# Kernel tuning notes

Measured on AMD Instinct MI355X. Metric: run time of the kernel, lower is better.

The kernel has to match this reference:

```python
import jax, jax.numpy as jnp
import numpy as np

SQRT_HALF = np.float32(np.sqrt(0.5))


def _weight_norm(v, g):
    # torch weight_norm dim=0: per-output-row normalization, w = g * v / ||v||_row
    return (g / jnp.linalg.norm(v, axis=1))[:, None] * v


def setup_inputs() -> dict:
    key = jax.random.key(0)
    ks = jax.random.split(key, 6)
    B, L, C, E, H, W = 32, 1024, 1024, 1024, 14, 14
    return {
        "x": jax.random.normal(ks[0], (B, L, C), dtype=jnp.float32),
        "word_embed": jax.random.normal(ks[1], (B, L, E), dtype=jnp.float32),
        "conv_feats": jax.random.normal(ks[2], (B, E, H, W), dtype=jnp.float32),
        "in_v": jax.random.normal(ks[3], (E, C), dtype=jnp.float32) * np.float32(1.0 / np.sqrt(C)),
        "in_g": jnp.ones((E,), dtype=jnp.float32),
        "in_b": jnp.zeros((E,), dtype=jnp.float32),
        "out_v": jax.random.normal(ks[4], (C, E), dtype=jnp.float32) * np.float32(1.0 / np.sqrt(E)),
        "out_g": jnp.ones((C,), dtype=jnp.float32),
        "out_b": jnp.zeros((C,), dtype=jnp.float32),
    }


def reference(x, word_embed, conv_feats, in_v, in_g, in_b, out_v, out_g, out_b):
    # in_projection (weight-normed linear) + word_embed, scaled
    Wi = _weight_norm(in_v, in_g)                      # [E, C]
    h = (jnp.einsum('blc,ec->ble', x, Wi) + in_b + word_embed) * SQRT_HALF  # [B, L, E]

    B, E, H, W = conv_feats.shape
    n = H * W
    y = conv_feats.reshape(B, E, n)                    # [B, E, n]
    scores = jnp.einsum('ble,bev->blv', h, y)          # [B, L, n]
    attn = jax.nn.softmax(scores, axis=-1)             # [B, L, n]
    ctx = jnp.einsum('blv,bev->ble', attn, y)          # [B, L, E]
    ctx = ctx * jnp.asarray(n * np.sqrt(1.0 / n), dtype=ctx.dtype)  # = sqrt(n)

    # out_projection + residual, scaled
    Wo = _weight_norm(out_v, out_g)                    # [C, E]
    out = (jnp.einsum('ble,ce->blc', ctx, Wo) + out_b + x) * SQRT_HALF  # [B, L, C]
    return out, attn
```

## Files before the change

### kernel.cpp

```cpp
#include <hip/hip_runtime.h>
#include <hip/hip_bf16.h>

typedef unsigned short u16;
typedef _Float16 f16x8 __attribute__((ext_vector_type(8)));
typedef unsigned short u16x8 __attribute__((ext_vector_type(8)));
typedef float f32x4 __attribute__((ext_vector_type(4)));

#define SQHF 0.70710678118654752440f

__device__ __forceinline__ u16 f2h(float f) {
  const _Float16 h = (_Float16)f;
  return __builtin_bit_cast(u16, h);
}

template <int N>
__device__ __forceinline__ void vmwait() {
  asm volatile("s_waitcnt vmcnt(%0)" ::"i"(N) : "memory");
}

__device__ __forceinline__ void gload_lds16(const void* g, void* l) {
  __builtin_amdgcn_global_load_lds(
      (const __attribute__((address_space(1))) unsigned int*)g,
      (__attribute__((address_space(3))) unsigned int*)l, 16, 0, 0);
}

__device__ __forceinline__ float block_sum(float v) {
#pragma unroll
  for (int o = 32; o; o >>= 1) v += __shfl_xor(v, o);
  __shared__ float red[4];
  if ((threadIdx.x & 63) == 0) red[threadIdx.x >> 6] = v;
  __syncthreads();
  return red[0] + red[1] + red[2] + red[3];
}

__global__ void wnorm_t_kernel(const float* __restrict__ v, const float* __restrict__ g,
                               u16* __restrict__ wtf) {
  const int e = blockIdx.x;
  const float* vr = v + (long)e * 1024;
  float ss = 0.f;
  for (int c = threadIdx.x; c < 1024; c += 256) { float t = vr[c]; ss += t * t; }
  const float tot = block_sum(ss);
  const float scl = g[e] / sqrtf(tot);
  for (int c = threadIdx.x; c < 1024; c += 256) wtf[(long)c * 1024 + e] = f2h(vr[c] * scl);
}

__global__ void wnorm_kernel(const float* __restrict__ v, const float* __restrict__ g,
                             u16* __restrict__ w) {
  const int c = blockIdx.x;
  const float* vr = v + (long)c * 1024;
  float ss = 0.f;
  for (int e = threadIdx.x; e < 1024; e += 256) { float t = vr[e]; ss += t * t; }
  const float tot = block_sum(ss);
  const float scl = g[c] / sqrtf(tot);
  for (int e = threadIdx.x; e < 1024; e += 256) w[(long)c * 1024 + e] = f2h(vr[e] * scl);
}

__global__ void prep_y_kernel(const float* __restrict__ conv, const float* __restrict__ in_b,
                              u16* __restrict__ concat, float* __restrict__ rc) {
  const int b = blockIdx.x >> 4;
  const int e0 = (blockIdx.x & 15) << 6;
  __shared__ float tile[64 * 224];
  const float* cb = conv + ((long)b * 1024 + e0) * 196;
  for (int idx = threadIdx.x; idx < 64 * 224; idx += 256) {
    const int rr = idx / 224, vv = idx - rr * 224;
    tile[idx] = (vv < 196) ? cb[(long)rr * 196 + vv] : 0.f;
  }
  __syncthreads();
  for (int idx = threadIdx.x; idx < 256 * 64; idx += 256) {
    const int vr = idx >> 6, c = idx & 63;
    const float val = (vr < 224) ? tile[c * 224 + vr] : 0.f;
    concat[((long)b * 256 + vr) * 2048 + 1024 + e0 + c] = f2h(val);
  }
  const int v = threadIdx.x;
  if (v < 196) {
    float s = 0.f;
#pragma unroll 8
    for (int rr = 0; rr < 64; ++rr) s += in_b[e0 + rr] * tile[rr * 224 + v];
    atomicAdd(&rc[b * 256 + v], s);
  }
}

__global__ void softmax_kernel(const float* __restrict__ s0b, const float* __restrict__ s1b,
                               const float* __restrict__ rc,
                               float* __restrict__ attn, u16* __restrict__ attn_f) {
  const long row = (long)blockIdx.x * 4 + (threadIdx.x >> 6);
  const int lane = threadIdx.x & 63;
  const int b = (int)(row >> 10);
  const float* s0 = s0b + row * 256;
  const float* s1 = s1b + row * 256;
  const float* rcb = rc + b * 256;
  float v0 = (s0[lane] + s1[lane] + rcb[lane]) * SQHF;
  float v1 = (s0[64 + lane] + s1[64 + lane] + rcb[64 + lane]) * SQHF;
  float v2 = (s0[128 + lane] + s1[128 + lane] + rcb[128 + lane]) * SQHF;
  float v3 = (lane < 4) ? (s0[192 + lane] + s1[192 + lane] + rcb[192 + lane]) * SQHF : -1e30f;
  float mx = fmaxf(fmaxf(v0, v1), fmaxf(v2, v3));
#pragma unroll
  for (int o = 32; o; o >>= 1) mx = fmaxf(mx, __shfl_xor(mx, o));
  const float e0 = __expf(v0 - mx), e1 = __expf(v1 - mx), e2 = __expf(v2 - mx);
  const float e3 = (lane < 4) ? __expf(v3 - mx) : 0.f;
  float sm = e0 + e1 + e2 + e3;
#pragma unroll
  for (int o = 32; o; o >>= 1) sm += __shfl_xor(sm, o);
  const float inv = 1.f / sm;
  float* arow = attn + row * 196;
  arow[lane] = e0 * inv;
  arow[64 + lane] = e1 * inv;
  arow[128 + lane] = e2 * inv;
  if (lane < 4) arow[192 + lane] = e3 * inv;
  u16* brow = attn_f + row * 256;
  brow[lane] = f2h(e0 * inv);
  brow[64 + lane] = f2h(e1 * inv);
  brow[128 + lane] = f2h(e2 * inv);
  brow[192 + lane] = (lane < 4) ? f2h(e3 * inv) : (u16)0;
}

template <int EPI, int MODE>
__global__ __launch_bounds__(256) void gemm128(
    const u16* __restrict__ Ah,
    const float* __restrict__ Af0, const float* __restrict__ Af1, int kSw,
    const u16* __restrict__ Bh,
    int N, int K, int ldA, int ldB, int ldOut,
    int mTilesPerBatch, long bStride, int aTilesMod, int kSplit2,
    const float* __restrict__ bias, const float* __restrict__ extra,
    float scale, void* __restrict__ out1, void* __restrict__ out2) {
  constexpr int AF32 = (MODE == 2);
  constexpr int LPS = AF32 ? 6 : 4;
  constexpr int TBH = AF32 ? 8192 : 4096;
  constexpr int HSM = AF32 ? 12288 : 8192;
  __shared__ __align__(16) u16 smem[HSM * 2];

  int bid = blockIdx.x, nwg = gridDim.x, half = 0;
  if (kSplit2) { half = bid & 1; bid >>= 1; nwg >>= 1; }
  const int kOff = half << 10;

  const int numN = N >> 7;
  const int q = nwg >> 3, r = nwg & 7, xcd = bid & 7, l8 = bid >> 3;
  const int wg = (xcd < r ? xcd * (q + 1) : r * (q + 1) + (xcd - r) * q) + l8;
  const int mTile = wg / numN, nTile = wg - mTile * numN;
  const long rowBase = (long)mTile << 7;
  const int colBase = nTile << 7;
  const int aTile = aTilesMod ? (mTile % aTilesMod) : mTile;
  const long aRowBase = (long)aTile << 7;
  const long bOff = mTilesPerBatch ? (long)(mTile / mTilesPerBatch) * bStride : 0;

  const u16* Agh = AF32 ? nullptr : (Ah + aRowBase * ldA);
  const u16* Bgh = Bh + bOff + (long)colBase * ldB;

  const int tid = threadIdx.x;
  const int wave = tid >> 6, lane = tid & 63;
  const int wr = wave >> 1, wc = wave & 1;
  const int sr = wave * 16 + (lane >> 2);
  const int scS = (((lane & 3) ^ ((sr >> 1) & 3)) << 3);
  const int lr = lane & 15;
  const int lk = (lane >> 4) << 3;

  f32x4 acc[4][4];
#pragma unroll
  for (int m = 0; m < 4; ++m)
#pragma unroll
    for (int n = 0; n < 4; ++n) acc[m][n] = f32x4{0.f, 0.f, 0.f, 0.f};

  auto stage = [&](int buf, int k0) {
    u16* sb = smem + buf * HSM;
    if (AF32) {
      const int gk = k0 + kOff;
      const float* As = (gk < kSw) ? (Af0 + aRowBase * (long)ldA + gk)
                                   : (Af1 + aRowBase * (long)ldA + (gk - kSw));
      const int rr = tid >> 3;
#pragma unroll
      for (int i = 0; i < 4; ++i) {
        const int row = i * 32 + rr;
        const int csw = (((tid & 7) ^ (row & 7)) << 2);
        gload_lds16(As + (long)row * ldA + csw, &sb[i * 2048 + wave * 512]);
      }
#pragma unroll
      for (int i = 0; i < 2; ++i) {
        const long ro = (long)(i * 64 + sr) * ldB + k0 + kOff + scS;
        gload_lds16(Bgh + ro, &sb[TBH + i * 2048 + wave * 512]);
      }
    } else {
#pragma unroll
      for (int i = 0; i < 2; ++i) {
        const long roA = (long)(i * 64 + sr) * ldA + k0 + kOff + scS;
        const long roB = (long)(i * 64 + sr) * ldB + k0 + kOff + scS;
        const int lo_ = i * 2048 + wave * 512;
        gload_lds16(Agh + roA, &sb[lo_]);
        gload_lds16(Bgh + roB, &sb[TBH + lo_]);
      }
    }
  };

  auto compute = [&](int buf) {
    const u16* sb = smem + buf * HSM;
    f16x8 fa[4], fb[4];
    if (AF32) {
      const char* smemb = (const char*)sb;
#pragma unroll
      for (int m = 0; m < 4; ++m) {
        const int row = wr * 64 + m * 16 + lr;
        const int xr = (row & 7) << 4;
        const char* rp = smemb + row * 128;
        const f32x4 p0 = *(const f32x4*)(rp + ((lk << 2) ^ xr));
        const f32x4 p1 = *(const f32x4*)(rp + (((lk << 2) + 16) ^ xr));
        f16x8 va;
        va[0] = (_Float16)p0.x; va[1] = (_Float16)p0.y;
        va[2] = (_Float16)p0.z; va[3] = (_Float16)p0.w;
        va[4] = (_Float16)p1.x; va[5] = (_Float16)p1.y;
        va[6] = (_Float16)p1.z; va[7] = (_Float16)p1.w;
        fa[m] = va;
      }
    } else {
#pragma unroll
      for (int m = 0; m < 4; ++m) {
        const int row = wr * 64 + m * 16 + lr;
        const int off = row * 32 + (((lane >> 4) ^ ((row >> 1) & 3)) << 3);
        fa[m] = __builtin_bit_cast(f16x8, *(const u16x8*)&sb[off]);
      }
    }
#pragma unroll
    for (int n = 0; n < 4; ++n) {
      const int row = wc * 64 + n * 16 + lr;
      const int off = row * 32 + (((lane >> 4) ^ ((row >> 1) & 3)) << 3);
      fb[n] = __builtin_bit_cast(f16x8, *(const u16x8*)&sb[TBH + off]);
    }
    __builtin_amdgcn_s_setprio(1);
#pragma unroll
    for (int m = 0; m < 4; ++m)
#pragma unroll
      for (int n = 0; n < 4; ++n)
        acc[m][n] = __builtin_amdgcn_mfma_f32_16x16x32_f16(fa[m], fb[n], acc[m][n], 0, 0, 0);
    __builtin_amdgcn_s_setprio(0);
  };

  const int nSteps = K >> 5;
  stage(0, 0);
  for (int t = 0; t < nSteps; ++t) {
    const int cur = t & 1;
    if (t + 1 < nSteps) {
      stage(cur ^ 1, (t + 1) << 5);
      vmwait<LPS>();
    } else {
      vmwait<0>();
    }
    __builtin_amdgcn_s_barrier();
    __builtin_amdgcn_sched_barrier(0);
    compute(cur);
    __builtin_amdgcn_sched_barrier(0);
    __builtin_amdgcn_s_barrier();
  }

  const int rloc = (lane >> 4) << 2;
  float* o3 = (float*)(half ? out2 : out1);
#pragma unroll
  for (int m = 0; m < 4; ++m) {
#pragma unroll
    for (int n = 0; n < 4; ++n) {
      const int col = colBase + wc * 64 + n * 16 + lr;
#pragma unroll
      for (int j = 0; j < 4; ++j) {
        const long row = rowBase + wr * 64 + m * 16 + rloc + j;
        const float v = acc[m][n][j];
        if (EPI == 1) {
          ((float*)out1)[row * (long)ldOut + col] =
              (v + bias[col] + extra[row * (long)ldOut + col]) * scale;
        } else if (EPI == 3) {
          o3[row * (long)ldOut + col] = v;
        } else if (EPI == 6) {
          ((u16*)out1)[row * (long)ldOut + col] = f2h(v * scale);
        }
      }
    }
  }
}

extern "C" void kernel_launch(void* const* d_in, const int* in_sizes, int n_in,
                              void* d_out, int out_size, void* d_ws, size_t ws_size,
                              hipStream_t stream) {
  (void)in_sizes; (void)n_in; (void)out_size; (void)ws_size;
  const float* x     = (const float*)d_in[0];
  const float* we    = (const float*)d_in[1];
  const float* conv  = (const float*)d_in[2];
  const float* in_v  = (const float*)d_in[3];
  const float* in_g  = (const float*)d_in[4];
  const float* in_b  = (const float*)d_in[5];
  const float* out_v = (const float*)d_in[6];
  const float* out_g = (const float*)d_in[7];
  const float* out_b = (const float*)d_in[8];
  float* out  = (float*)d_out;
  float* attn = out + 33554432l;

  char* ws = (char*)d_ws;
  u16* concat = (u16*)(ws);
  u16* wtf    = (u16*)(ws + 33554432l);
  u16* wo     = (u16*)(ws + 35651584l);
  u16* zo     = (u16*)(ws + 37748736l);
  u16* attf   = (u16*)(ws + 54525952l);
  float* rc   = (float*)(ws + 71303168l);
  float* s1   = (float*)(ws + 71368704l);
  float* s0   = out;

  hipMemsetAsync(rc, 0, 32 * 256 * sizeof(float), stream);
  wnorm_t_kernel<<<1024, 256, 0, stream>>>(in_v, in_g, wtf);
  wnorm_kernel<<<1024, 256, 0, stream>>>(out_v, out_g, wo);
  prep_y_kernel<<<512, 256, 0, stream>>>(conv, in_b, concat, rc);
  gemm128<6, 3><<<512, 256, 0, stream>>>(
      concat + 1024, nullptr, nullptr, 0, wtf,
      1024, 1024, 2048, 1024, 2048, 0, 0, 0, 0, nullptr, nullptr, 1.f, concat, nullptr);
  gemm128<3, 2><<<1024, 256, 0, stream>>>(
      nullptr, x, we, 1024, concat,
      256, 1024, 1024, 2048, 256, 8, 524288l, 0, 1, nullptr, nullptr, 1.f, s0, s1);
  softmax_kernel<<<8192, 256, 0, stream>>>(s0, s1, rc, attn, attf);
  gemm128<6, 3><<<512, 256, 0, stream>>>(
      wo, nullptr, nullptr, 0, concat + 1024,
      256, 1024, 1024, 2048, 256, 8, 524288l, 8, 0, nullptr, nullptr, 14.f, zo, nullptr);
  gemm128<1, 3><<<2048, 256, 0, stream>>>(
      attf, nullptr, nullptr, 0, zo,
      1024, 256, 256, 256, 1024, 8, 262144l, 0, 0, out_b, x, SQHF, out, nullptr);
}
```

Baseline: 302.1 us.

## Stage fp32 A operand through registers with fp16 conversion before LDS write

For the fp32-input GEMM mode, A tiles are now loaded from global memory into registers, converted to fp16 there, and written to LDS as half precision. Previously the raw fp32 data went to LDS by direct global-to-LDS loads and was converted on every fragment read. This halves the LDS footprint and read traffic for A and removes conversion work from the MFMA inner loop. The cost is a more complex software pipeline with register-staged prefetch two steps ahead and manual waitcnt bookkeeping, which raises register pressure and makes the synchronisation more fragile.

```diff
diff --git a/kernel.cpp b/kernel.cpp
--- a/kernel.cpp
+++ b/kernel.cpp
@@ -123,10 +123,9 @@
     int mTilesPerBatch, long bStride, int aTilesMod, int kSplit2,
     const float* __restrict__ bias, const float* __restrict__ extra,
     float scale, void* __restrict__ out1, void* __restrict__ out2) {
-  constexpr int AF32 = (MODE == 2);
-  constexpr int LPS = AF32 ? 6 : 4;
-  constexpr int TBH = AF32 ? 8192 : 4096;
-  constexpr int HSM = AF32 ? 12288 : 8192;
+  constexpr int AREG = (MODE == 2);
+  constexpr int TBH = 4096;
+  constexpr int HSM = 8192;
   __shared__ __align__(16) u16 smem[HSM * 2];
 
   int bid = blockIdx.x, nwg = gridDim.x, half = 0;
@@ -143,7 +142,7 @@
   const long aRowBase = (long)aTile << 7;
   const long bOff = mTilesPerBatch ? (long)(mTile / mTilesPerBatch) * bStride : 0;
 
-  const u16* Agh = AF32 ? nullptr : (Ah + aRowBase * ldA);
+  const u16* Agh = AREG ? nullptr : (Ah + aRowBase * ldA);
   const u16* Bgh = Bh + bOff + (long)colBase * ldB;
 
   const int tid = threadIdx.x;
@@ -152,7 +151,6 @@
   const int sr = wave * 16 + (lane >> 2);
   const int scS = (((lane & 3) ^ ((sr >> 1) & 3)) << 3);
   const int lr = lane & 15;
-  const int lk = (lane >> 4) << 3;
 
   f32x4 acc[4][4];
 #pragma unroll
@@ -160,62 +158,31 @@
 #pragma unroll
     for (int n = 0; n < 4; ++n) acc[m][n] = f32x4{0.f, 0.f, 0.f, 0.f};
 
-  auto stage = [&](int buf, int k0) {
+  auto stageB = [&](int buf, int k0) {
     u16* sb = smem + buf * HSM;
-    if (AF32) {
-      const int gk = k0 + kOff;
-      const float* As = (gk < kSw) ? (Af0 + aRowBase * (long)ldA + gk)
-                                   : (Af1 + aRowBase * (long)ldA + (gk - kSw));
-      const int rr = tid >> 3;
-#pragma unroll
-      for (int i = 0; i < 4; ++i) {
-        const int row = i * 32 + rr;
-        const int csw = (((tid & 7) ^ (row & 7)) << 2);
-        gload_lds16(As + (long)row * ldA + csw, &sb[i * 2048 + wave * 512]);
-      }
-#pragma unroll
-      for (int i = 0; i < 2; ++i) {
-        const long ro = (long)(i * 64 + sr) * ldB + k0 + kOff + scS;
-        gload_lds16(Bgh + ro, &sb[TBH + i * 2048 + wave * 512]);
-      }
-    } else {
-#pragma unroll
-      for (int i = 0; i < 2; ++i) {
-        const long roA = (long)(i * 64 + sr) * ldA + k0 + kOff + scS;
-        const long roB = (long)(i * 64 + sr) * ldB + k0 + kOff + scS;
-        const int lo_ = i * 2048 + wave * 512;
-        gload_lds16(Agh + roA, &sb[lo_]);
-        gload_lds16(Bgh + roB, &sb[TBH + lo_]);
-      }
+#pragma unroll
+    for (int i = 0; i < 2; ++i) {
+      const long ro = (long)(i * 64 + sr) * ldB + k0 + kOff + scS;
+      gload_lds16(Bgh + ro, &sb[TBH + i * 2048 + wave * 512]);
+    }
+  };
+  auto stageA_lds = [&](int buf, int k0) {
+    u16* sb = smem + buf * HSM;
+#pragma unroll
+    for (int i = 0; i < 2; ++i) {
+      const long ro = (long)(i * 64 + sr) * ldA + k0 + kOff + scS;
+      gload_lds16(Agh + ro, &sb[i * 2048 + wave * 512]);
     }
   };
 
   auto compute = [&](int buf) {
     const u16* sb = smem + buf * HSM;
     f16x8 fa[4], fb[4];
-    if (AF32) {
-      const char* smemb = (const char*)sb;
-#pragma unroll
-      for (int m = 0; m < 4; ++m) {
-        const int row = wr * 64 + m * 16 + lr;
-        const int xr = (row & 7) << 4;
-        const char* rp = smemb + row * 128;
-        const f32x4 p0 = *(const f32x4*)(rp + ((lk << 2) ^ xr));
-        const f32x4 p1 = *(const f32x4*)(rp + (((lk << 2) + 16) ^ xr));
-        f16x8 va;
-        va[0] = (_Float16)p0.x; va[1] = (_Float16)p0.y;
-        va[2] = (_Float16)p0.z; va[3] = (_Float16)p0.w;
-        va[4] = (_Float16)p1.x; va[5] = (_Float16)p1.y;
-        va[6] = (_Float16)p1.z; va[7] = (_Float16)p1.w;
-        fa[m] = va;
-      }
-    } else {
-#pragma unroll
-      for (int m = 0; m < 4; ++m) {
-        const int row = wr * 64 + m * 16 + lr;
-        const int off = row * 32 + (((lane >> 4) ^ ((row >> 1) & 3)) << 3);
-        fa[m] = __builtin_bit_cast(f16x8, *(const u16x8*)&sb[off]);
-      }
+#pragma unroll
+    for (int m = 0; m < 4; ++m) {
+      const int row = wr * 64 + m * 16 + lr;
+      const int off = row * 32 + (((lane >> 4) ^ ((row >> 1) & 3)) << 3);
+      fa[m] = __builtin_bit_cast(f16x8, *(const u16x8*)&sb[off]);
     }
 #pragma unroll
     for (int n = 0; n < 4; ++n) {
@@ -233,20 +200,70 @@
   };
 
   const int nSteps = K >> 5;
-  stage(0, 0);
-  for (int t = 0; t < nSteps; ++t) {
-    const int cur = t & 1;
-    if (t + 1 < nSteps) {
-      stage(cur ^ 1, (t + 1) << 5);
-      vmwait<LPS>();
-    } else {
-      vmwait<0>();
-    }
-    __builtin_amdgcn_s_barrier();
-    __builtin_amdgcn_sched_barrier(0);
-    compute(cur);
-    __builtin_amdgcn_sched_barrier(0);
-    __builtin_amdgcn_s_barrier();
+
+  if constexpr (AREG) {
+    const int arow = tid >> 2, akch = tid & 3;
+    const int r1 = arow + 64;
+    const int aoff0 = arow * 32 + ((akch ^ ((arow >> 1) & 3)) << 3);
+    const int aoff1 = r1 * 32 + ((akch ^ ((r1 >> 1) & 3)) << 3);
+    f32x4 ra0, ra1, rb0, rb1;
+    auto issueA = [&](int k0) {
+      const int gk = k0 + kOff;
+      const float* As = (gk < kSw) ? (Af0 + aRowBase * (long)ldA + gk)
+                                   : (Af1 + aRowBase * (long)ldA + (gk - kSw));
+      const float* p0 = As + (long)arow * ldA + akch * 8;
+      const float* p1 = As + (long)r1 * ldA + akch * 8;
+      ra0 = *(const f32x4*)p0; ra1 = *(const f32x4*)(p0 + 4);
+      rb0 = *(const f32x4*)p1; rb1 = *(const f32x4*)(p1 + 4);
+    };
+    auto writeA = [&](int buf) {
+      u16* sb = smem + buf * HSM;
+      u16x8 w0, w1;
+      w0[0] = f2h(ra0[0]); w0[1] = f2h(ra0[1]); w0[2] = f2h(ra0[2]); w0[3] = f2h(ra0[3]);
+      w0[4] = f2h(ra1[0]); w0[5] = f2h(ra1[1]); w0[6] = f2h(ra1[2]); w0[7] = f2h(ra1[3]);
+      w1[0] = f2h(rb0[0]); w1[1] = f2h(rb0[1]); w1[2] = f2h(rb0[2]); w1[3] = f2h(rb0[3]);
+      w1[4] = f2h(rb1[0]); w1[5] = f2h(rb1[1]); w1[6] = f2h(rb1[2]); w1[7] = f2h(rb1[3]);
+      *(u16x8*)&sb[aoff0] = w0;
+      *(u16x8*)&sb[aoff1] = w1;
+    };
+    issueA(0); stageB(0, 0);
+    vmwait<2>();
+    writeA(0);
+    if (nSteps > 1) { issueA(32); stageB(1, 32); }
+    for (int t = 0; t < nSteps; ++t) {
+      if (t + 1 < nSteps) {
+        asm volatile("s_waitcnt vmcnt(6) lgkmcnt(0)" ::: "memory");
+      } else {
+        asm volatile("s_waitcnt vmcnt(0) lgkmcnt(0)" ::: "memory");
+      }
+      __builtin_amdgcn_s_barrier();
+      __builtin_amdgcn_sched_barrier(0);
+      compute(t & 1);
+      __builtin_amdgcn_sched_barrier(0);
+      __builtin_amdgcn_s_barrier();
+      if (t + 1 < nSteps) {
+        vmwait<2>();
+        writeA((t + 1) & 1);
+        if (t + 2 < nSteps) { issueA((t + 2) << 5); stageB(t & 1, (t + 2) << 5); }
+      }
+    }
+  } else {
+    stageA_lds(0, 0); stageB(0, 0);
+    for (int t = 0; t < nSteps; ++t) {
+      const int cur = t & 1;
+      if (t + 1 < nSteps) {
+        stageA_lds(cur ^ 1, (t + 1) << 5);
+        stageB(cur ^ 1, (t + 1) << 5);
+        vmwait<4>();
+      } else {
+        vmwait<0>();
+      }
+      __builtin_amdgcn_s_barrier();
+      __builtin_amdgcn_sched_barrier(0);
+      compute(cur);
+      __builtin_amdgcn_sched_barrier(0);
+      __builtin_amdgcn_s_barrier();
+    }
   }
 
   const int rloc = (lane >> 4) << 2;
```

Measured after the change: 307.5 us. About the same (+1.8%).

## Use 256-row M tiles for the fp32-A scores GEMM to halve B reloads

Applied to the files above, without the earlier changes.

For the MODE 2 GEMM, which reads x/word_embed as fp32 and computes scores, the M tile grows from 128 to 256 rows. Each wave now computes 8 M-fragments, and the launch shrinks to 512 workgroups with 4 m-tiles per batch. Each B (concat) tile is reused across twice as many rows, cutting B traffic and workgroup overhead. The cost is more LDS per block (double-buffered 40K halves), twice the accumulator registers, and fewer workgroups, which may lower occupancy and latency hiding.

```diff
diff --git a/kernel.cpp b/kernel.cpp
--- a/kernel.cpp
+++ b/kernel.cpp
@@ -124,9 +124,11 @@
     const float* __restrict__ bias, const float* __restrict__ extra,
     float scale, void* __restrict__ out1, void* __restrict__ out2) {
   constexpr int AF32 = (MODE == 2);
-  constexpr int LPS = AF32 ? 6 : 4;
-  constexpr int TBH = AF32 ? 8192 : 4096;
-  constexpr int HSM = AF32 ? 12288 : 8192;
+  constexpr int MROWS = AF32 ? 256 : 128;
+  constexpr int MFRAG = AF32 ? 8 : 4;
+  constexpr int LPS = AF32 ? 10 : 4;
+  constexpr int TBH = AF32 ? 16384 : 4096;
+  constexpr int HSM = AF32 ? 20480 : 8192;
   __shared__ __align__(16) u16 smem[HSM * 2];
 
   int bid = blockIdx.x, nwg = gridDim.x, half = 0;
@@ -137,10 +139,10 @@
   const int q = nwg >> 3, r = nwg & 7, xcd = bid & 7, l8 = bid >> 3;
   const int wg = (xcd < r ? xcd * (q + 1) : r * (q + 1) + (xcd - r) * q) + l8;
   const int mTile = wg / numN, nTile = wg - mTile * numN;
-  const long rowBase = (long)mTile << 7;
+  const long rowBase = (long)mTile * MROWS;
   const int colBase = nTile << 7;
   const int aTile = aTilesMod ? (mTile % aTilesMod) : mTile;
-  const long aRowBase = (long)aTile << 7;
+  const long aRowBase = (long)aTile * MROWS;
   const long bOff = mTilesPerBatch ? (long)(mTile / mTilesPerBatch) * bStride : 0;
 
   const u16* Agh = AF32 ? nullptr : (Ah + aRowBase * ldA);
@@ -154,9 +156,9 @@
   const int lr = lane & 15;
   const int lk = (lane >> 4) << 3;
 
-  f32x4 acc[4][4];
-#pragma unroll
-  for (int m = 0; m < 4; ++m)
+  f32x4 acc[MFRAG][4];
+#pragma unroll
+  for (int m = 0; m < MFRAG; ++m)
 #pragma unroll
     for (int n = 0; n < 4; ++n) acc[m][n] = f32x4{0.f, 0.f, 0.f, 0.f};
 
@@ -168,7 +170,7 @@
                                    : (Af1 + aRowBase * (long)ldA + (gk - kSw));
       const int rr = tid >> 3;
 #pragma unroll
-      for (int i = 0; i < 4; ++i) {
+      for (int i = 0; i < 8; ++i) {
         const int row = i * 32 + rr;
         const int csw = (((tid & 7) ^ (row & 7)) << 2);
         gload_lds16(As + (long)row * ldA + csw, &sb[i * 2048 + wave * 512]);
@@ -192,44 +194,57 @@
 
   auto compute = [&](int buf) {
     const u16* sb = smem + buf * HSM;
-    f16x8 fa[4], fb[4];
+    f16x8 fb[4];
+#pragma unroll
+    for (int n = 0; n < 4; ++n) {
+      const int row = wc * 64 + n * 16 + lr;
+      const int off = TBH + row * 32 + (((lane >> 4) ^ ((row >> 1) & 3)) << 3);
+      fb[n] = __builtin_bit_cast(f16x8, *(const u16x8*)&sb[off]);
+    }
     if (AF32) {
       const char* smemb = (const char*)sb;
 #pragma unroll
-      for (int m = 0; m < 4; ++m) {
-        const int row = wr * 64 + m * 16 + lr;
-        const int xr = (row & 7) << 4;
-        const char* rp = smemb + row * 128;
-        const f32x4 p0 = *(const f32x4*)(rp + ((lk << 2) ^ xr));
-        const f32x4 p1 = *(const f32x4*)(rp + (((lk << 2) + 16) ^ xr));
-        f16x8 va;
-        va[0] = (_Float16)p0.x; va[1] = (_Float16)p0.y;
-        va[2] = (_Float16)p0.z; va[3] = (_Float16)p0.w;
-        va[4] = (_Float16)p1.x; va[5] = (_Float16)p1.y;
-        va[6] = (_Float16)p1.z; va[7] = (_Float16)p1.w;
-        fa[m] = va;
+      for (int h = 0; h < 2; ++h) {
+        f16x8 fa[4];
+#pragma unroll
+        for (int m = 0; m < 4; ++m) {
+          const int row = wr * 128 + (h * 4 + m) * 16 + lr;
+          const int xr = (row & 7) << 4;
+          const char* rp = smemb + row * 128;
+          const f32x4 p0 = *(const f32x4*)(rp + ((lk << 2) ^ xr));
+          const f32x4 p1 = *(const f32x4*)(rp + (((lk << 2) + 16) ^ xr));
+          f16x8 va;
+          va[0] = (_Float16)p0.x; va[1] = (_Float16)p0.y;
+          va[2] = (_Float16)p0.z; va[3] = (_Float16)p0.w;
+          va[4] = (_Float16)p1.x; va[5] = (_Float16)p1.y;
+          va[6] = (_Float16)p1.z; va[7] = (_Float16)p1.w;
+          fa[m] = va;
+        }
+        __builtin_amdgcn_s_setprio(1);
+#pragma unroll
+        for (int m = 0; m < 4; ++m)
+#pragma unroll
+          for (int n = 0; n < 4; ++n)
+            acc[h * 4 + m][n] =
+                __builtin_amdgcn_mfma_f32_16x16x32_f16(fa[m], fb[n], acc[h * 4 + m][n], 0, 0, 0);
+        __builtin_amdgcn_s_setprio(0);
       }
     } else {
+      f16x8 fa[4];
 #pragma unroll
       for (int m = 0; m < 4; ++m) {
         const int row = wr * 64 + m * 16 + lr;
         const int off = row * 32 + (((lane >> 4) ^ ((row >> 1) & 3)) << 3);
         fa[m] = __builtin_bit_cast(f16x8, *(const u16x8*)&sb[off]);
       }
-    }
-#pragma unroll
-    for (int n = 0; n < 4; ++n) {
-      const int row = wc * 64 + n * 16 + lr;
-      const int off = row * 32 + (((lane >> 4) ^ ((row >> 1) & 3)) << 3);
-      fb[n] = __builtin_bit_cast(f16x8, *(const u16x8*)&sb[TBH + off]);
-    }
-    __builtin_amdgcn_s_setprio(1);
-#pragma unroll
-    for (int m = 0; m < 4; ++m)
-#pragma unroll
-      for (int n = 0; n < 4; ++n)
-        acc[m][n] = __builtin_amdgcn_mfma_f32_16x16x32_f16(fa[m], fb[n], acc[m][n], 0, 0, 0);
-    __builtin_amdgcn_s_setprio(0);
+      __builtin_amdgcn_s_setprio(1);
+#pragma unroll
+      for (int m = 0; m < 4; ++m)
+#pragma unroll
+        for (int n = 0; n < 4; ++n)
+          acc[m][n] = __builtin_amdgcn_mfma_f32_16x16x32_f16(fa[m], fb[n], acc[m][n], 0, 0, 0);
+      __builtin_amdgcn_s_setprio(0);
+    }
   };
 
   const int nSteps = K >> 5;
@@ -252,13 +267,13 @@
   const int rloc = (lane >> 4) << 2;
   float* o3 = (float*)(half ? out2 : out1);
 #pragma unroll
-  for (int m = 0; m < 4; ++m) {
+  for (int m = 0; m < MFRAG; ++m) {
 #pragma unroll
     for (int n = 0; n < 4; ++n) {
       const int col = colBase + wc * 64 + n * 16 + lr;
 #pragma unroll
       for (int j = 0; j < 4; ++j) {
-        const long row = rowBase + wr * 64 + m * 16 + rloc + j;
+        const long row = rowBase + wr * (MROWS / 2) + m * 16 + rloc + j;
         const float v = acc[m][n][j];
         if (EPI == 1) {
           ((float*)out1)[row * (long)ldOut + col] =
@@ -306,9 +321,9 @@
   gemm128<6, 3><<<512, 256, 0, stream>>>(
       concat + 1024, nullptr, nullptr, 0, wtf,
       1024, 1024, 2048, 1024, 2048, 0, 0, 0, 0, nullptr, nullptr, 1.f, concat, nullptr);
-  gemm128<3, 2><<<1024, 256, 0, stream>>>(
+  gemm128<3, 2><<<512, 256, 0, stream>>>(
       nullptr, x, we, 1024, concat,
-      256, 1024, 1024, 2048, 256, 8, 524288l, 0, 1, nullptr, nullptr, 1.f, s0, s1);
+      256, 1024, 1024, 2048, 256, 4, 524288l, 0, 1, nullptr, nullptr, 1.f, s0, s1);
   softmax_kernel<<<8192, 256, 0, stream>>>(s0, s1, rc, attn, attf);
   gemm128<6, 3><<<512, 256, 0, stream>>>(
       wo, nullptr, nullptr, 0, concat + 1024,
```

Measured after the change: 304.2 us. Within noise of the previous version (+0.7%).
